# Optimization experiments

Measured on AMD Instinct MI355X. Metric: run time of the kernel, lower is better.

The kernel has to match this reference:

```python
import jax, jax.numpy as jnp
import numpy as np

Tx, V, D = 512, 100, 64
DM, NH, DFF, NL = 512, 8, 2048, 2
H, DATT, FCH, OUT = 256, 128, 256, 2


def setup_inputs() -> dict:
    key = jax.random.key(0)
    ks = jax.random.split(key, 16)
    s = 0.02
    w = lambda k, shape: jax.random.normal(k, shape, jnp.float32) * s
    return dict(
        x_data=jax.random.normal(ks[0], (1, Tx, V, D), jnp.float32),
        feat_w=w(ks[1], (DM, D)), feat_b=jnp.zeros((DM,), jnp.float32),
        in_w=w(ks[2], (NL, 3 * DM, DM)), in_b=jnp.zeros((NL, 3 * DM), jnp.float32),
        out_w=w(ks[3], (NL, DM, DM)), out_b=jnp.zeros((NL, DM), jnp.float32),
        ff1_w=w(ks[4], (NL, DFF, DM)), ff1_b=jnp.zeros((NL, DFF), jnp.float32),
        ff2_w=w(ks[5], (NL, DM, DFF)), ff2_b=jnp.zeros((NL, DM), jnp.float32),
        ln1_g=jnp.ones((NL, DM), jnp.float32), ln1_b=jnp.zeros((NL, DM), jnp.float32),
        ln2_g=jnp.ones((NL, DM), jnp.float32), ln2_b=jnp.zeros((NL, DM), jnp.float32),
        att1_w=w(ks[6], (DATT, DM + H)), att1_b=jnp.zeros((DATT,), jnp.float32),
        att2_w=w(ks[7], (1, DATT)), att2_b=jnp.zeros((1,), jnp.float32),
        lstm_wih=w(ks[8], (4 * H, DM)), lstm_whh=w(ks[9], (4 * H, H)),
        lstm_bih=jnp.zeros((4 * H,), jnp.float32), lstm_bhh=jnp.zeros((4 * H,), jnp.float32),
        fc1_w=w(ks[10], (FCH, DM + H)), fc1_b=jnp.zeros((FCH,), jnp.float32),
        fc2_w=w(ks[11], (OUT, FCH)), fc2_b=jnp.zeros((OUT,), jnp.float32),
    )


def _layernorm(x, g, b):
    m = x.mean(-1, keepdims=True)
    v = x.var(-1, keepdims=True)
    return (x - m) * jax.lax.rsqrt(v + 1e-5) * g + b


def _forward(x_data, feat_w, feat_b, in_w, in_b, out_w, out_b, ff1_w, ff1_b,
             ff2_w, ff2_b, ln1_g, ln1_b, ln2_g, ln2_b, att1_w, att1_b,
             att2_w, att2_b, lstm_wih, lstm_whh, lstm_bih, lstm_bhh,
             fc1_w, fc1_b, fc2_w, fc2_b):
    x = x_data[0]                              # [Tx, V, D]
    x = jnp.swapaxes(x, 0, 1)                  # [V, Tx, D]  (seq=V, batch=Tx)
    x = x @ feat_w.T + feat_b                  # feature mapping -> [V, Tx, DM]
    # sinusoidal positional encoding over the V (seq) axis
    pos = jnp.arange(V, dtype=jnp.float32)[:, None]
    div = jnp.exp(jnp.arange(0, DM, 2, dtype=jnp.float32) * (-np.log(10000.0) / DM))
    pe = jnp.zeros((V, DM), jnp.float32)
    pe = pe.at[:, 0::2].set(jnp.sin(pos * div)).at[:, 1::2].set(jnp.cos(pos * div))
    x = x + pe[:, None, :]
    hd = DM // NH
    for l in range(NL):                        # post-norm TransformerEncoderLayer
        qkv = x @ in_w[l].T + in_b[l]          # [V, Tx, 3*DM]
        q, k, v = jnp.split(qkv, 3, axis=-1)
        q = q.reshape(V, Tx, NH, hd)
        k = k.reshape(V, Tx, NH, hd)
        v = v.reshape(V, Tx, NH, hd)
        scores = jnp.einsum('ibhd,jbhd->bhij', q, k) / np.sqrt(hd).astype(np.float32)
        attn = jax.nn.softmax(scores, axis=-1)
        ctx = jnp.einsum('bhij,jbhd->ibhd', attn, v).reshape(V, Tx, DM)
        x = _layernorm(x + ctx @ out_w[l].T + out_b[l], ln1_g[l], ln1_b[l])
        ff = jax.nn.relu(x @ ff1_w[l].T + ff1_b[l]) @ ff2_w[l].T + ff2_b[l]
        x = _layernorm(x + ff, ln2_g[l], ln2_b[l])
    hs = jnp.swapaxes(x, 0, 1)                 # [Tx, V, DM]

    def step(carry, h_i):                      # h_i: [V, DM]
        s_h, s_c = carry                       # [1, H] each
        att_in = jnp.concatenate([h_i, jnp.broadcast_to(s_h, (V, H))], axis=1)
        a1 = jnp.tanh(att_in @ att1_w.T + att1_b)
        a2 = a1 @ att2_w.T + att2_b            # [V, 1]
        a2 = a2 - jnp.max(a2)
        alpha = jnp.exp(a2)
        alpha = alpha / (jnp.sum(alpha, axis=0, keepdims=True) + 1e-15)
        c = jnp.sum(alpha * h_i, axis=0, keepdims=True)   # [1, DM]
        gates = c @ lstm_wih.T + lstm_bih + s_h @ lstm_whh.T + lstm_bhh
        i_g, f_g, g_g, o_g = jnp.split(gates, 4, axis=-1)
        s_c_new = jax.nn.sigmoid(f_g) * s_c + jax.nn.sigmoid(i_g) * jnp.tanh(g_g)
        s_h_new = jax.nn.sigmoid(o_g) * jnp.tanh(s_c_new)
        fc_in = jnp.concatenate([c, s_h], axis=1)  # uses PREVIOUS hidden, per original
        fc = jax.nn.relu(fc_in @ fc1_w.T + fc1_b) @ fc2_w.T + fc2_b
        log_prob = jax.nn.log_softmax(fc, axis=1)  # [1, OUT]
        return (s_h_new, s_c_new), log_prob

    init = (jnp.zeros((1, H), jnp.float32), jnp.zeros((1, H), jnp.float32))
    _, logs = jax.lax.scan(step, init, hs)
    return logs[-1]                            # last timestep's log-probs [1, OUT]


def reference(x_data, feat_w, feat_b, in_w, in_b, out_w, out_b, ff1_w, ff1_b,
              ff2_w, ff2_b, ln1_g, ln1_b, ln2_g, ln2_b, att1_w, att1_b,
              att2_w, att2_b, lstm_wih, lstm_whh, lstm_bih, lstm_bhh,
              fc1_w, fc1_b, fc2_w, fc2_b):
    return _forward(x_data, feat_w, feat_b, in_w, in_b, out_w, out_b, ff1_w,
                    ff1_b, ff2_w, ff2_b, ln1_g, ln1_b, ln2_g, ln2_b, att1_w,
                    att1_b, att2_w, att2_b, lstm_wih, lstm_whh, lstm_bih,
                    lstm_bhh, fc1_w, fc1_b, fc2_w, fc2_b)
```

## Files before the change

kernel.cpp:

```cpp
#include <hip/hip_runtime.h>
#include <hip/hip_bf16.h>


typedef __attribute__((ext_vector_type(8))) short short8;
typedef __attribute__((ext_vector_type(4))) float f32x4;

__device__ __forceinline__ int jglob_of(int e0, int jl) { return ((jl >> 4) << 8) + e0 + (jl & 15); }
__device__ __forceinline__ float blo(unsigned u) { return __uint_as_float(u << 16); }
__device__ __forceinline__ float bhi(unsigned u) { return __uint_as_float(u & 0xffff0000u); }
__device__ __forceinline__ short f2bs(float x) {
  union { __hip_bfloat16 h; short s; } u; u.h = __float2bfloat16(x); return u.s;
}
__device__ __forceinline__ float tanhf_fast(float x) {
  float e = __expf(2.f * x);
  return 1.f - 2.f * __builtin_amdgcn_rcpf(e + 1.f);
}

#define GLL16(GSRC, LDST) \
  __builtin_amdgcn_global_load_lds( \
      (const __attribute__((address_space(1))) unsigned int*)(GSRC), \
      (__attribute__((address_space(3))) unsigned int*)(LDST), 16, 0, 0)

__global__ __launch_bounds__(256) void pe_kernel(float* __restrict__ pe) {
  int idx = blockIdx.x * 256 + threadIdx.x;
  if (idx >= 100 * 512) return;
  int v = idx >> 9, n = idx & 511;
  float d = expf(-(float)(n & ~1) * (9.2103403719761836f / 512.0f));
  float ang = (float)v * d;
  pe[idx] = (n & 1) ? cosf(ang) : sinf(ang);
}

__global__ __launch_bounds__(256) void cvt_kernel(const float* __restrict__ src,
                                                  __hip_bfloat16* __restrict__ dst, int n) {
  int i = blockIdx.x * 256 + threadIdx.x;
  if (i < n) dst[i] = __float2bfloat16(src[i]);
}

__global__ __launch_bounds__(256) void gemm_bf16(
    const __hip_bfloat16* __restrict__ A, long aBase, int aDiv, long aSA, long aSB,
    const __hip_bfloat16* __restrict__ W, int ldw,
    const float* __restrict__ bias,
    float* __restrict__ outF, __hip_bfloat16* __restrict__ outB,
    long oBase, int oDiv, long oSA, long oSB,
    int K, int addTo, int relu)
{
  __shared__ __hip_bfloat16 As[128 * 64];
  __shared__ __hip_bfloat16 Bs[128 * 64];
  const int tid = threadIdx.x;
  const int rT = blockIdx.y * 128, nT = blockIdx.x * 128;
  const int wave = tid >> 6, lane = tid & 63;
  const int wr = wave >> 1, wc = wave & 1;
  const int lrow = lane & 15, lkg = lane >> 4;

  long asrc[4], bsrc[4];
  const int sc8 = ((lane & 7) ^ (lane >> 3)) * 8;
#pragma unroll
  for (int i = 0; i < 4; ++i) {
    const int chunk = wave * 4 + i;
    const int row = chunk * 8 + (lane >> 3);
    const int gr = rT + row;
    asrc[i] = aBase + (long)(gr / aDiv) * aSA + (long)(gr % aDiv) * aSB + sc8;
    bsrc[i] = (long)(nT + row) * ldw + sc8;
  }

  f32x4 acc[4][4];
#pragma unroll
  for (int i = 0; i < 4; ++i)
#pragma unroll
    for (int j = 0; j < 4; ++j) acc[i][j] = (f32x4){0.f, 0.f, 0.f, 0.f};

  for (int k0 = 0; k0 < K; k0 += 64) {
#pragma unroll
    for (int i = 0; i < 4; ++i) {
      const int chunk = wave * 4 + i;
      GLL16(A + asrc[i] + k0, &As[chunk * 512]);
      GLL16(W + bsrc[i] + k0, &Bs[chunk * 512]);
    }
    __syncthreads();
#pragma unroll
    for (int ks = 0; ks < 2; ++ks) {
      short8 af[4], bfv[4];
#pragma unroll
      for (int f = 0; f < 4; ++f) {
        const int Ra = wr * 64 + f * 16 + lrow;
        af[f] = *(const short8*)&As[Ra * 64 + (((ks * 4 + lkg) ^ (Ra & 7)) * 8)];
        const int Rb = wc * 64 + f * 16 + lrow;
        bfv[f] = *(const short8*)&Bs[Rb * 64 + (((ks * 4 + lkg) ^ (Rb & 7)) * 8)];
      }
#pragma unroll
      for (int fm = 0; fm < 4; ++fm)
#pragma unroll
        for (int fn = 0; fn < 4; ++fn)
          acc[fm][fn] = __builtin_amdgcn_mfma_f32_16x16x32_bf16(af[fm], bfv[fn], acc[fm][fn], 0, 0, 0);
    }
    __syncthreads();
  }

  float bias_v[4];
#pragma unroll
  for (int fn = 0; fn < 4; ++fn)
    bias_v[fn] = bias ? bias[nT + wc * 64 + fn * 16 + lrow] : 0.f;

#pragma unroll
  for (int fm = 0; fm < 4; ++fm) {
#pragma unroll
    for (int r = 0; r < 4; ++r) {
      const int grow = rT + wr * 64 + fm * 16 + lkg * 4 + r;
      const long obase_r = oBase + (long)(grow / oDiv) * oSA + (long)(grow % oDiv) * oSB;
#pragma unroll
      for (int fn = 0; fn < 4; ++fn) {
        const int gcol = nT + wc * 64 + fn * 16 + lrow;
        float v = acc[fm][fn][r] + bias_v[fn];
        if (relu) v = fmaxf(v, 0.f);
        const long o = obase_r + gcol;
        if (outF) { if (addTo) v += outF[o]; outF[o] = v; }
        else outB[o] = __float2bfloat16(v);
      }
    }
  }
}

__global__ __launch_bounds__(256) void gemm_mfma(
    const float* __restrict__ A, long aBase, int aDiv, long aSA, long aSB,
    const float* __restrict__ W, int ldw,
    const float* __restrict__ bias,
    const float* __restrict__ extra, int extraDiv,
    float* __restrict__ outF, __hip_bfloat16* __restrict__ outB,
    __hip_bfloat16* __restrict__ outB2,
    long oBase, int oDiv, long oSA, long oSB, long oSC,
    int N, int K, int addTo, int relu)
{
  __shared__ short As[2][128][40];
  __shared__ short Bs[2][128][40];
  const int tid = threadIdx.x;
  const int rT = blockIdx.y * 128, nT = blockIdx.x * 128;
  const int wave = tid >> 6, lane = tid & 63;
  const int wr = wave >> 1, wc = wave & 1;
  const int lrow = lane & 15, lkg = lane >> 4;
  const int srow = tid >> 1, shf = tid & 1;

  const long arow = aBase + (long)((rT + srow) / aDiv) * aSA + (long)((rT + srow) % aDiv) * aSB + shf * 16;
  const long brow = (long)(nT + srow) * ldw + shf * 16;

  f32x4 acc[4][4];
#pragma unroll
  for (int i = 0; i < 4; ++i)
#pragma unroll
    for (int j = 0; j < 4; ++j) acc[i][j] = (f32x4){0.f, 0.f, 0.f, 0.f};

  float4 ra[4], rb[4];
#define LOADT(K0) do { \
    const float* _pa = A + arow + (K0); \
    ra[0] = *(const float4*)(_pa); ra[1] = *(const float4*)(_pa + 4); \
    ra[2] = *(const float4*)(_pa + 8); ra[3] = *(const float4*)(_pa + 12); \
    const float* _pb = W + brow + (K0); \
    rb[0] = *(const float4*)(_pb); rb[1] = *(const float4*)(_pb + 4); \
    rb[2] = *(const float4*)(_pb + 8); rb[3] = *(const float4*)(_pb + 12); \
  } while (0)

#define CVST(DST, X, Y) do { \
    short8 _v; \
    _v[0] = f2bs((X).x); _v[1] = f2bs((X).y); _v[2] = f2bs((X).z); _v[3] = f2bs((X).w); \
    _v[4] = f2bs((Y).x); _v[5] = f2bs((Y).y); _v[6] = f2bs((Y).z); _v[7] = f2bs((Y).w); \
    *(short8*)(DST) = _v; \
  } while (0)

#define STAGE(BUF) do { \
    CVST(&As[BUF][srow][shf * 16],     ra[0], ra[1]); \
    CVST(&As[BUF][srow][shf * 16 + 8], ra[2], ra[3]); \
    CVST(&Bs[BUF][srow][shf * 16],     rb[0], rb[1]); \
    CVST(&Bs[BUF][srow][shf * 16 + 8], rb[2], rb[3]); \
  } while (0)

  LOADT(0);
  STAGE(0);
  __syncthreads();

  int cur = 0;
  for (int k0 = 0; k0 < K; k0 += 32) {
    const bool nlast = (k0 + 32 < K);
    if (nlast) LOADT(k0 + 32);
    short8 af[4], bfv[4];
#pragma unroll
    for (int f = 0; f < 4; ++f)
      af[f] = *(const short8*)&As[cur][wr * 64 + f * 16 + lrow][lkg * 8];
#pragma unroll
    for (int f = 0; f < 4; ++f)
      bfv[f] = *(const short8*)&Bs[cur][wc * 64 + f * 16 + lrow][lkg * 8];
#pragma unroll
    for (int fm = 0; fm < 4; ++fm)
#pragma unroll
      for (int fn = 0; fn < 4; ++fn)
        acc[fm][fn] = __builtin_amdgcn_mfma_f32_16x16x32_bf16(af[fm], bfv[fn], acc[fm][fn], 0, 0, 0);
    if (nlast) STAGE(cur ^ 1);
    __syncthreads();
    cur ^= 1;
  }

  float bias_v[4];
#pragma unroll
  for (int fn = 0; fn < 4; ++fn)
    bias_v[fn] = bias ? bias[nT + wc * 64 + fn * 16 + lrow] : 0.f;

#pragma unroll
  for (int fm = 0; fm < 4; ++fm) {
#pragma unroll
    for (int r = 0; r < 4; ++r) {
      const int grow = rT + wr * 64 + fm * 16 + lkg * 4 + r;
      const long obase_r = oBase + (long)(grow / oDiv) * oSA + (long)(grow % oDiv) * oSB;
      const long exrow = (long)(grow / extraDiv) * N;
#pragma unroll
      for (int fn = 0; fn < 4; ++fn) {
        const int gcol = nT + wc * 64 + fn * 16 + lrow;
        float v = acc[fm][fn][r] + bias_v[fn];
        if (extra) v += extra[exrow + gcol];
        if (relu) v = fmaxf(v, 0.f);
        const long o = obase_r + (long)gcol * oSC;
        if (outF) { if (addTo) v += outF[o]; outF[o] = v; }
        else outB[o] = __float2bfloat16(v);
        if (outB2) outB2[o] = __float2bfloat16(v);
      }
    }
  }
#undef LOADT
#undef CVST
#undef STAGE
}

__global__ __launch_bounds__(256) void attn_kernel(
    const __hip_bfloat16* __restrict__ qkv, __hip_bfloat16* __restrict__ outY)
{
  __shared__ __align__(16) char arena[101632];
  unsigned short* Qs = (unsigned short*)arena;
  unsigned short* Ks = Qs + 8064;
  unsigned short* Vt = Ks + 8064;
  float* S = (float*)(arena + 49664);
  unsigned short* Sb = (unsigned short*)arena;
  __shared__ float rs_s[112];

  const int h = blockIdx.x, bl = blockIdx.y, tid = threadIdx.x;
  const unsigned short* q16 = (const unsigned short*)qkv;

  for (int idx = tid; idx < 6400; idx += 256) {
    int v = idx >> 6, d = idx & 63;
    long base = ((long)(v * 128 + bl)) * 1536 + h * 64 + d;
    Qs[v * 72 + d] = q16[base];
    Ks[v * 72 + d] = q16[base + 512];
    Vt[d * 136 + v] = q16[base + 1024];
  }
  for (int idx = tid; idx < 12 * 64; idx += 256) {
    int r = 100 + (idx >> 6), c = idx & 63;
    Qs[r * 72 + c] = 0; Ks[r * 72 + c] = 0;
  }
  for (int idx = tid; idx < 64 * 36; idx += 256) {
    int d = idx / 36, c = 100 + idx % 36;
    Vt[d * 136 + c] = 0;
  }
  __syncthreads();

  const int wave = tid >> 6, lane = tid & 63;
  const int lrow = lane & 15, lkg = lane >> 4;

  for (int tt = wave; tt < 49; tt += 4) {
    const int tm = tt / 7, tn = tt % 7;
    f32x4 a = (f32x4){0.f, 0.f, 0.f, 0.f};
#pragma unroll
    for (int ks = 0; ks < 2; ++ks) {
      short8 af = *(const short8*)&Qs[(tm * 16 + lrow) * 72 + ks * 32 + lkg * 8];
      short8 bf = *(const short8*)&Ks[(tn * 16 + lrow) * 72 + ks * 32 + lkg * 8];
      a = __builtin_amdgcn_mfma_f32_16x16x32_bf16(af, bf, a, 0, 0, 0);
    }
#pragma unroll
    for (int r = 0; r < 4; ++r)
      S[(tm * 16 + lkg * 4 + r) * 116 + tn * 16 + lrow] = a[r] * 0.125f;
  }
  __syncthreads();

  {
    unsigned* p = (unsigned*)Sb;
    for (int idx = tid; idx < 7616; idx += 256) p[idx] = 0;
  }
  __syncthreads();

  if (tid < 200) {
    const int r = tid >> 1, hf = tid & 1;
    const float* srow = S + r * 116 + hf * 50;
    float m = -3.0e38f;
    for (int c = 0; c < 50; ++c) m = fmaxf(m, srow[c]);
    m = fmaxf(m, __shfl_xor(m, 1, 64));
    float s = 0.f;
    for (int c = 0; c < 50; ++c) {
      float e = __expf(srow[c] - m);
      Sb[r * 136 + hf * 50 + c] = (unsigned short)f2bs(e);
      s += e;
    }
    s += __shfl_xor(s, 1, 64);
    if (hf == 0) rs_s[r] = 1.f / s;
  }
  __syncthreads();

  for (int tt = wave; tt < 28; tt += 4) {
    const int tm = tt >> 2, tn = tt & 3;
    f32x4 a = (f32x4){0.f, 0.f, 0.f, 0.f};
#pragma unroll
    for (int kc = 0; kc < 4; ++kc) {
      short8 af = *(const short8*)&Sb[(tm * 16 + lrow) * 136 + kc * 32 + lkg * 8];
      short8 bf = *(const short8*)&Vt[(tn * 16 + lrow) * 136 + kc * 32 + lkg * 8];
      a = __builtin_amdgcn_mfma_f32_16x16x32_bf16(af, bf, a, 0, 0, 0);
    }
#pragma unroll
    for (int r = 0; r < 4; ++r) {
      const int m = tm * 16 + lkg * 4 + r;
      if (m < 100) {
        const int n = tn * 16 + lrow;
        outY[((long)m * 128 + bl) * 512 + h * 64 + n] = __float2bfloat16(a[r] * rs_s[m]);
      }
    }
  }
}

__global__ __launch_bounds__(256) void ln_kernel(float* __restrict__ X,
    __hip_bfloat16* __restrict__ Xb,
    const float* __restrict__ g, const float* __restrict__ b)
{
  const int row = blockIdx.x * 4 + (threadIdx.x >> 6);
  const int lane = threadIdx.x & 63;
  float* x = X + (long)row * 512;
  __hip_bfloat16* xb = Xb + (long)row * 512;
  float v[8]; float s = 0.f, sq = 0.f;
#pragma unroll
  for (int i = 0; i < 8; ++i) { v[i] = x[lane + i * 64]; s += v[i]; sq += v[i] * v[i]; }
#pragma unroll
  for (int off = 32; off; off >>= 1) { s += __shfl_xor(s, off, 64); sq += __shfl_xor(sq, off, 64); }
  const float mean = s * (1.f / 512.f);
  const float var = sq * (1.f / 512.f) - mean * mean;
  const float inv = rsqrtf(var + 1e-5f);
#pragma unroll
  for (int i = 0; i < 8; ++i) {
    int c = lane + i * 64;
    float r = (v[i] - mean) * inv * g[c] + b[c];
    x[c] = r;
    xb[c] = __float2bfloat16(r);
  }
}

__global__ void init_kernel(unsigned long long* sh_units, float* c_g) {
  int t = threadIdx.x;
  sh_units[t] = 0ULL;
  sh_units[256 + t] = 0ULL;
  c_g[t] = 0.f; c_g[256 + t] = 0.f;
}

#define DEC_NB 16

__global__ __launch_bounds__(256, 1) void decoder_kernel(
    const float* __restrict__ X,
    const __hip_bfloat16* __restrict__ Pb,
    const __hip_bfloat16* __restrict__ Gb,
    const float* __restrict__ att1_w, const float* __restrict__ att1_b,
    const float* __restrict__ att2_w,
    const float* __restrict__ whh,
    const float* __restrict__ bih, const float* __restrict__ bhh,
    const float* __restrict__ fc1_w, const float* __restrict__ fc1_b,
    const float* __restrict__ fc2_w, const float* __restrict__ fc2_b,
    unsigned long long* sh_units,
    float* c_g,
    float* __restrict__ out)
{
  if (blockIdx.x & 7) return;
  const int tid = threadIdx.x;
  const int blk = blockIdx.x >> 3;
  const int e0 = blk * 16;

  __shared__ __align__(16) float s_h_s[256];
  __shared__ float w2_s[128], ub_s[128], bsum_s[64];
  __shared__ float u_s[128], sc_s[16];
  __shared__ float a2_s[104];
  __shared__ float red_s[256];
  __shared__ float gates_s[64];
  __shared__ float red4_s[4];
  __shared__ float fcin_s[768];
  __shared__ float fca_s[256];

  if (tid < 128) { w2_s[tid] = att2_w[tid]; ub_s[tid] = att1_b[tid]; }
  if (tid < 64) {
    int jg = jglob_of(e0, tid);
    bsum_s[tid] = bih[jg] + bhh[jg];
  }
  if (tid < 16) sc_s[tid] = 0.f;
  if (tid < 4) a2_s[100 + tid] = 0.f;

  const int pv = tid >> 1, ppart = tid & 1;
  const int pvv = (pv < 100) ? pv : 99;
  const int gjl = tid >> 2, gq = tid & 3;
  const long gRowOff = (long)jglob_of(e0, gjl) * 100 + gq * 26;

  unsigned W1R[64];
  {
    const int j = tid >> 1, hf = tid & 1;
    const float* wsrc = att1_w + (long)j * 768 + 512 + hf * 128;
#pragma unroll
    for (int i = 0; i < 64; ++i)
      W1R[i] = (unsigned)(unsigned short)f2bs(wsrc[2 * i]) |
               ((unsigned)(unsigned short)f2bs(wsrc[2 * i + 1]) << 16);
  }
  float WHF[64];
  {
    const float* wsrc = whh + (long)jglob_of(e0, gjl) * 256 + gq * 64;
#pragma unroll
    for (int i = 0; i < 64; ++i) WHF[i] = wsrc[i];
  }

  unsigned PCa[32], PCb[32];
  unsigned GCa[13], GCb[13];

#define PREFETCH(T1, PCd, GCd) do { \
    const uint4* _pp = (const uint4*)Pb + ((((long)(T1) * 100 + pvv) * 128 + ppart * 64) >> 3); \
    _Pragma("unroll") \
    for (int _i = 0; _i < 8; ++_i) { \
      uint4 _t = _pp[_i]; \
      (PCd)[4*_i] = _t.x; (PCd)[4*_i+1] = _t.y; (PCd)[4*_i+2] = _t.z; (PCd)[4*_i+3] = _t.w; \
    } \
    const unsigned* _gp = (const unsigned*)(Gb + (long)(T1) * 102400 + gRowOff); \
    _Pragma("unroll") \
    for (int _i = 0; _i < 13; ++_i) (GCd)[_i] = _gp[_i]; \
  } while (0)

#define STEP(T, PCc, GCc, PCn, GCn) do { \
     \
    { \
      unsigned long long* _up = &sh_units[((((T) & 1) ^ 1) << 8) + tid]; \
      unsigned long long _v = __hip_atomic_load(_up, __ATOMIC_RELAXED, __HIP_MEMORY_SCOPE_AGENT); \
      while ((unsigned)(_v >> 32) < (unsigned)(T)) { \
        __builtin_amdgcn_s_sleep(1); \
        _v = __hip_atomic_load(_up, __ATOMIC_RELAXED, __HIP_MEMORY_SCOPE_AGENT); \
      } \
      s_h_s[tid] = __uint_as_float((unsigned)_v); \
    } \
    __syncthreads(); \
     \
    if ((T) + 1 < 512) PREFETCH((T) + 1, PCn, GCn); \
     \
    { const int _hf = tid & 1, _j = tid >> 1; \
      const float* _sh = &s_h_s[_hf * 128]; \
      float _a = 0.f; \
      _Pragma("unroll") \
      for (int _i = 0; _i < 64; ++_i) { \
        const unsigned _w = W1R[_i]; \
        const float2 _s2 = *(const float2*)(_sh + 2 * _i); \
        _a += blo(_w) * _s2.x + bhi(_w) * _s2.y; \
      } \
      _a += __shfl_xor(_a, 1, 64); \
      if (_hf == 0) u_s[_j] = _a + ub_s[_j]; \
    } \
    float _hhv; \
    { const float* _sh = &s_h_s[gq * 64]; \
      float _a = 0.f; \
      _Pragma("unroll") \
      for (int _i = 0; _i < 16; ++_i) { \
        const float4 _s4 = *(const float4*)(_sh + 4 * _i); \
        _a += WHF[4*_i] * _s4.x + WHF[4*_i+1] * _s4.y + WHF[4*_i+2] * _s4.z + WHF[4*_i+3] * _s4.w; \
      } \
      _a += __shfl_xor(_a, 1, 64); \
      _a += __shfl_xor(_a, 2, 64); \
      _hhv = _a; \
    } \
    __syncthreads(); \
     \
    { float _val = 0.f; \
      _Pragma("unroll") \
      for (int _jj = 0; _jj < 64; ++_jj) { \
        unsigned _u = (PCc)[_jj >> 1]; \
        float _pf = (_jj & 1) ? bhi(_u) : blo(_u); \
        int _col = ppart * 64 + _jj; \
        _val += tanhf_fast(_pf + u_s[_col]) * w2_s[_col]; \
      } \
      _val += __shfl_xor(_val, 1, 64); \
      if (ppart == 0 && pv < 100) a2_s[pv] = _val; \
    } \
    __syncthreads(); \
     \
    if (tid < 64) { \
      float _x0 = a2_s[tid]; \
      float _x1 = (tid + 64 < 100) ? a2_s[tid + 64] : -3.0e38f; \
      float _m = fmaxf(_x0, _x1); \
      _Pragma("unroll") \
      for (int _o = 32; _o; _o >>= 1) _m = fmaxf(_m, __shfl_xor(_m, _o, 64)); \
      float _e0 = __expf(_x0 - _m); \
      float _e1 = (tid + 64 < 100) ? __expf(_x1 - _m) : 0.f; \
      float _s = _e0 + _e1; \
      _Pragma("unroll") \
      for (int _o = 32; _o; _o >>= 1) _s += __shfl_xor(_s, _o, 64); \
      const float _inv = 1.f / (_s + 1e-15f); \
      a2_s[tid] = _e0 * _inv; \
      if (tid + 64 < 100) a2_s[tid + 64] = _e1 * _inv; \
    } \
    __syncthreads(); \
     \
    { float _p = 0.f; \
      _Pragma("unroll") \
      for (int _i = 0; _i < 13; ++_i) { \
        unsigned _u = (GCc)[_i]; \
        _p += a2_s[gq * 26 + 2 * _i] * blo(_u); \
        _p += a2_s[gq * 26 + 2 * _i + 1] * bhi(_u); \
      } \
      _p += __shfl_xor(_p, 1, 64); \
      _p += __shfl_xor(_p, 2, 64); \
      if (gq == 0) gates_s[gjl] = _p + _hhv + bsum_s[gjl]; \
    } \
    __syncthreads(); \
     \
    if ((T) < 511) { \
      if (tid < 16) { \
        const float _ig = gates_s[tid], _fg = gates_s[16 + tid]; \
        const float _gg = gates_s[32 + tid], _og = gates_s[48 + tid]; \
        const float _si = 1.f / (1.f + __expf(-_ig)); \
        const float _sf = 1.f / (1.f + __expf(-_fg)); \
        const float _so = 1.f / (1.f + __expf(-_og)); \
        const float _sc = _sf * sc_s[tid] + _si * tanhf(_gg); \
        sc_s[tid] = _sc; \
        const float _sh2 = _so * tanhf(_sc); \
        const unsigned long long _v = \
            ((unsigned long long)(unsigned)((T) + 1) << 32) | (unsigned long long)__float_as_uint(_sh2); \
        __hip_atomic_store(&sh_units[(((T) & 1) << 8) + e0 + tid], _v, \
                           __ATOMIC_RELAXED, __HIP_MEMORY_SCOPE_AGENT); \
      } \
    } else { \
      const int _dl = tid & 31, _vs = tid >> 5; \
      const int _v0 = _vs * 13, _v1 = (_v0 + 13 < 100) ? _v0 + 13 : 100; \
      float _ac = 0.f; \
      for (int _v = _v0; _v < _v1; ++_v) \
        _ac += a2_s[_v] * X[((long)(_v * 512 + 511)) * 512 + blk * 32 + _dl]; \
      red_s[tid] = _ac; \
      __syncthreads(); \
      if (tid < 32) { \
        float _cc = 0.f; \
        _Pragma("unroll") \
        for (int _s = 0; _s < 8; ++_s) _cc += red_s[_s * 32 + tid]; \
        __hip_atomic_store(&c_g[blk * 32 + tid], _cc, __ATOMIC_RELAXED, __HIP_MEMORY_SCOPE_AGENT); \
      } \
      __syncthreads(); \
      if (tid == 0) \
        __hip_atomic_store(&sh_units[256 + e0], 512ULL << 32, \
                           __ATOMIC_RELEASE, __HIP_MEMORY_SCOPE_AGENT); \
    } \
  } while (0)

  PREFETCH(0, PCa, GCa);
  __syncthreads();

  for (int t2 = 0; t2 < 512; t2 += 2) {
    STEP(t2,     PCa, GCa, PCb, GCb);
    STEP(t2 + 1, PCb, GCb, PCa, GCa);
  }

  if (blk == 0) {
    if (tid < DEC_NB) {
      while ((unsigned)(__hip_atomic_load(&sh_units[256 + tid * 16],
                 __ATOMIC_RELAXED, __HIP_MEMORY_SCOPE_AGENT) >> 32) < 512u)
        __builtin_amdgcn_s_sleep(1);
    }
    __builtin_amdgcn_fence(__ATOMIC_ACQUIRE, "agent");
    __syncthreads();
    fcin_s[tid]       = __hip_atomic_load(&c_g[tid],       __ATOMIC_RELAXED, __HIP_MEMORY_SCOPE_AGENT);
    fcin_s[256 + tid] = __hip_atomic_load(&c_g[256 + tid], __ATOMIC_RELAXED, __HIP_MEMORY_SCOPE_AGENT);
    fcin_s[512 + tid] = s_h_s[tid];
    __syncthreads();
    float acc = fc1_b[tid];
    const float* w = fc1_w + (long)tid * 768;
    for (int k = 0; k < 768; ++k) acc += w[k] * fcin_s[k];
    fca_s[tid] = fmaxf(acc, 0.f);
    __syncthreads();
    if (tid < 128) {
      const int r = tid >> 6, k0 = tid & 63;
      float a = 0.f;
#pragma unroll
      for (int s = 0; s < 4; ++s) a += fc2_w[r * 256 + k0 + s * 64] * fca_s[k0 + s * 64];
#pragma unroll
      for (int off = 32; off; off >>= 1) a += __shfl_xor(a, off, 64);
      if (k0 == 0) red4_s[r] = a + fc2_b[r];
    }
    __syncthreads();
    if (tid == 0) {
      const float l0 = red4_s[0], l1 = red4_s[1];
      const float m = fmaxf(l0, l1);
      const float ls = logf(__expf(l0 - m) + __expf(l1 - m));
      out[0] = l0 - m - ls;
      out[1] = l1 - m - ls;
    }
  }
#undef PREFETCH
#undef STEP
}

extern "C" void kernel_launch(void* const* d_in, const int* in_sizes, int n_in,
                              void* d_out, int out_size, void* d_ws, size_t ws_size,
                              hipStream_t stream) {
  const float* x_data  = (const float*)d_in[0];
  const float* feat_w  = (const float*)d_in[1];
  const float* feat_b  = (const float*)d_in[2];
  const float* in_w    = (const float*)d_in[3];
  const float* in_b    = (const float*)d_in[4];
  const float* out_w   = (const float*)d_in[5];
  const float* out_b   = (const float*)d_in[6];
  const float* ff1_w   = (const float*)d_in[7];
  const float* ff1_b   = (const float*)d_in[8];
  const float* ff2_w   = (const float*)d_in[9];
  const float* ff2_b   = (const float*)d_in[10];
  const float* ln1_g   = (const float*)d_in[11];
  const float* ln1_b   = (const float*)d_in[12];
  const float* ln2_g   = (const float*)d_in[13];
  const float* ln2_b   = (const float*)d_in[14];
  const float* att1_w  = (const float*)d_in[15];
  const float* att1_b  = (const float*)d_in[16];
  const float* att2_w  = (const float*)d_in[17];
  const float* lstm_wih = (const float*)d_in[19];
  const float* lstm_whh = (const float*)d_in[20];
  const float* lstm_bih = (const float*)d_in[21];
  const float* lstm_bhh = (const float*)d_in[22];
  const float* fc1_w   = (const float*)d_in[23];
  const float* fc1_b   = (const float*)d_in[24];
  const float* fc2_w   = (const float*)d_in[25];
  const float* fc2_b   = (const float*)d_in[26];

  float* ws   = (float*)d_ws;
  float* Xf   = ws;
  float* R    = Xf + 26214400;
  __hip_bfloat16* Xb   = (__hip_bfloat16*)R;
  __hip_bfloat16* qkvb = (__hip_bfloat16*)(R + 13107200);
  __hip_bfloat16* ctxb = (__hip_bfloat16*)(R + 22937600);
  __hip_bfloat16* ffh  = (__hip_bfloat16*)(R + 13107200);
  __hip_bfloat16* wb   = (__hip_bfloat16*)(R + 26214400);
  __hip_bfloat16* in_wb  = wb;
  __hip_bfloat16* out_wb = wb + 1572864;
  __hip_bfloat16* ff1_wb = out_wb + 524288;
  __hip_bfloat16* ff2_wb = ff1_wb + 2097152;
  __hip_bfloat16* PbB = (__hip_bfloat16*)R;
  __hip_bfloat16* GbB = (__hip_bfloat16*)(R + 3276800);
  float* pe    = R + 29491200;
  unsigned long long* sh_units = (unsigned long long*)(pe + 51200);
  float* c_g   = (float*)(sh_units + 512);

  pe_kernel<<<200, 256, 0, stream>>>(pe);
  cvt_kernel<<<(1572864 + 255) / 256, 256, 0, stream>>>(in_w, in_wb, 1572864);
  cvt_kernel<<<(524288 + 255) / 256, 256, 0, stream>>>(out_w, out_wb, 524288);
  cvt_kernel<<<(2097152 + 255) / 256, 256, 0, stream>>>(ff1_w, ff1_wb, 2097152);
  cvt_kernel<<<(2097152 + 255) / 256, 256, 0, stream>>>(ff2_w, ff2_wb, 2097152);

  gemm_mfma<<<dim3(4, 400), 256, 0, stream>>>(
      x_data, 0L, 512, 64L, 6400L, feat_w, 64, feat_b, pe, 512,
      Xf, nullptr, Xb, 0L, 1 << 30, 0L, 512L, 1L, 512, 64, 0, 0);

  for (int l = 0; l < 2; ++l) {
    for (int c = 0; c < 4; ++c) {
      const long b0 = c * 128;
      gemm_bf16<<<dim3(12, 100), 256, 0, stream>>>(
          Xb, b0 * 512, 128, 262144L, 512L,
          in_wb + (long)l * 786432, 512, in_b + l * 1536,
          nullptr, qkvb, 0L, 1 << 30, 0L, 1536L, 512, 0, 0);
      attn_kernel<<<dim3(8, 128), 256, 0, stream>>>(qkvb, ctxb);
      gemm_bf16<<<dim3(4, 100), 256, 0, stream>>>(
          ctxb, 0L, 1 << 30, 0L, 512L,
          out_wb + (long)l * 262144, 512, out_b + l * 512,
          Xf, nullptr, b0 * 512, 128, 262144L, 512L, 512, 1, 0);
    }
    ln_kernel<<<12800, 256, 0, stream>>>(Xf, Xb, ln1_g + l * 512, ln1_b + l * 512);
    for (int rc = 0; rc < 4; ++rc) {
      const long r0 = (long)rc * 12800;
      gemm_bf16<<<dim3(16, 100), 256, 0, stream>>>(
          Xb, r0 * 512, 1 << 30, 0L, 512L,
          ff1_wb + (long)l * 1048576, 512, ff1_b + l * 2048,
          nullptr, ffh, 0L, 1 << 30, 0L, 2048L, 512, 0, 1);
      gemm_bf16<<<dim3(4, 100), 256, 0, stream>>>(
          ffh, 0L, 1 << 30, 0L, 2048L,
          ff2_wb + (long)l * 1048576, 2048, ff2_b + l * 512,
          Xf, nullptr, r0 * 512, 1 << 30, 0L, 512L, 2048, 1, 0);
    }
    ln_kernel<<<12800, 256, 0, stream>>>(Xf, Xb, ln2_g + l * 512, ln2_b + l * 512);
  }

  gemm_mfma<<<dim3(1, 400), 256, 0, stream>>>(
      Xf, 0L, 100, 512L, 262144L, att1_w, 768, nullptr, nullptr, 1,
      nullptr, PbB, nullptr, 0L, 1 << 30, 0L, 128L, 1L, 128, 512, 0, 0);
  gemm_mfma<<<dim3(8, 400), 256, 0, stream>>>(
      Xf, 0L, 100, 512L, 262144L, lstm_wih, 512, nullptr, nullptr, 1,
      nullptr, GbB, nullptr, 0L, 100, 102400L, 1L, 100L, 1024, 512, 0, 0);

  init_kernel<<<1, 256, 0, stream>>>(sh_units, c_g);
  decoder_kernel<<<DEC_NB * 8, 256, 0, stream>>>(
      Xf, PbB, GbB, att1_w, att1_b, att2_w,
      lstm_whh, lstm_bih, lstm_bhh, fc1_w, fc1_b, fc2_w, fc2_b,
      sh_units, c_g, (float*)d_out);
}
```

Before: 5.339 ms.

## Keep residual stream in bf16 only and batch attention/GEMM chunks larger

Removes the fp32 residual buffer so the whole encoder stream lives in bf16. Residual adds in the GEMM epilogues and layernorm now read and write bf16, with vectorized 16-byte layernorm access. Attention and FFN chunks double in size, the out-projection runs once per layer, and the post-encoder projections use the bf16 GEMM with pre-converted weights. This cuts memory traffic and launch count but adds bf16 rounding to every residual update, which may hurt accuracy.

```diff
diff --git a/kernel.cpp b/kernel.cpp
--- a/kernel.cpp
+++ b/kernel.cpp
@@ -30,10 +30,11 @@
   pe[idx] = (n & 1) ? cosf(ang) : sinf(ang);
 }
 
-__global__ __launch_bounds__(256) void cvt_kernel(const float* __restrict__ src,
-                                                  __hip_bfloat16* __restrict__ dst, int n) {
+__global__ __launch_bounds__(256) void cvt2_kernel(const float* __restrict__ src,
+                                                   __hip_bfloat16* __restrict__ dst,
+                                                   int n, int w, int stride) {
   int i = blockIdx.x * 256 + threadIdx.x;
-  if (i < n) dst[i] = __float2bfloat16(src[i]);
+  if (i < n) dst[i] = __float2bfloat16(src[(i / w) * stride + (i % w)]);
 }
 
 __global__ __launch_bounds__(256) void gemm_bf16(
@@ -41,7 +42,7 @@
     const __hip_bfloat16* __restrict__ W, int ldw,
     const float* __restrict__ bias,
     float* __restrict__ outF, __hip_bfloat16* __restrict__ outB,
-    long oBase, int oDiv, long oSA, long oSB,
+    long oBase, int oDiv, long oSA, long oSB, long oSC,
     int K, int addTo, int relu)
 {
   __shared__ __hip_bfloat16 As[128 * 64];
@@ -112,9 +113,12 @@
         const int gcol = nT + wc * 64 + fn * 16 + lrow;
         float v = acc[fm][fn][r] + bias_v[fn];
         if (relu) v = fmaxf(v, 0.f);
-        const long o = obase_r + gcol;
+        const long o = obase_r + (long)gcol * oSC;
         if (outF) { if (addTo) v += outF[o]; outF[o] = v; }
-        else outB[o] = __float2bfloat16(v);
+        else {
+          if (addTo) v += __bfloat162float(outB[o]);
+          outB[o] = __float2bfloat16(v);
+        }
       }
     }
   }
@@ -125,10 +129,9 @@
     const float* __restrict__ W, int ldw,
     const float* __restrict__ bias,
     const float* __restrict__ extra, int extraDiv,
-    float* __restrict__ outF, __hip_bfloat16* __restrict__ outB,
-    __hip_bfloat16* __restrict__ outB2,
-    long oBase, int oDiv, long oSA, long oSB, long oSC,
-    int N, int K, int addTo, int relu)
+    __hip_bfloat16* __restrict__ outB,
+    long oBase, int oDiv, long oSA, long oSB,
+    int N, int K)
 {
   __shared__ short As[2][128][40];
   __shared__ short Bs[2][128][40];
@@ -214,11 +217,7 @@
         const int gcol = nT + wc * 64 + fn * 16 + lrow;
         float v = acc[fm][fn][r] + bias_v[fn];
         if (extra) v += extra[exrow + gcol];
-        if (relu) v = fmaxf(v, 0.f);
-        const long o = obase_r + (long)gcol * oSC;
-        if (outF) { if (addTo) v += outF[o]; outF[o] = v; }
-        else outB[o] = __float2bfloat16(v);
-        if (outB2) outB2[o] = __float2bfloat16(v);
+        outB[obase_r + gcol] = __float2bfloat16(v);
       }
     }
   }
@@ -228,7 +227,7 @@
 }
 
 __global__ __launch_bounds__(256) void attn_kernel(
-    const __hip_bfloat16* __restrict__ qkv, __hip_bfloat16* __restrict__ outY)
+    const __hip_bfloat16* __restrict__ qkv, __hip_bfloat16* __restrict__ outY, int b0)
 {
   __shared__ __align__(16) char arena[101632];
   unsigned short* Qs = (unsigned short*)arena;
@@ -243,7 +242,7 @@
 
   for (int idx = tid; idx < 6400; idx += 256) {
     int v = idx >> 6, d = idx & 63;
-    long base = ((long)(v * 128 + bl)) * 1536 + h * 64 + d;
+    long base = ((long)(v * 256 + bl)) * 1536 + h * 64 + d;
     Qs[v * 72 + d] = q16[base];
     Ks[v * 72 + d] = q16[base + 512];
     Vt[d * 136 + v] = q16[base + 1024];
@@ -313,35 +312,36 @@
       const int m = tm * 16 + lkg * 4 + r;
       if (m < 100) {
         const int n = tn * 16 + lrow;
-        outY[((long)m * 128 + bl) * 512 + h * 64 + n] = __float2bfloat16(a[r] * rs_s[m]);
+        outY[((long)(m * 512 + b0 + bl)) * 512 + h * 64 + n] = __float2bfloat16(a[r] * rs_s[m]);
       }
     }
   }
 }
 
-__global__ __launch_bounds__(256) void ln_kernel(float* __restrict__ X,
-    __hip_bfloat16* __restrict__ Xb,
+__global__ __launch_bounds__(256) void ln_kernel(__hip_bfloat16* __restrict__ X,
     const float* __restrict__ g, const float* __restrict__ b)
 {
   const int row = blockIdx.x * 4 + (threadIdx.x >> 6);
   const int lane = threadIdx.x & 63;
-  float* x = X + (long)row * 512;
-  __hip_bfloat16* xb = Xb + (long)row * 512;
-  float v[8]; float s = 0.f, sq = 0.f;
-#pragma unroll
-  for (int i = 0; i < 8; ++i) { v[i] = x[lane + i * 64]; s += v[i]; sq += v[i] * v[i]; }
+  unsigned short* x = (unsigned short*)X + (long)row * 512 + lane * 8;
+  uint4 raw = *(const uint4*)x;
+  float v[8];
+  v[0] = blo(raw.x); v[1] = bhi(raw.x); v[2] = blo(raw.y); v[3] = bhi(raw.y);
+  v[4] = blo(raw.z); v[5] = bhi(raw.z); v[6] = blo(raw.w); v[7] = bhi(raw.w);
+  float s = 0.f, sq = 0.f;
+#pragma unroll
+  for (int i = 0; i < 8; ++i) { s += v[i]; sq += v[i] * v[i]; }
 #pragma unroll
   for (int off = 32; off; off >>= 1) { s += __shfl_xor(s, off, 64); sq += __shfl_xor(sq, off, 64); }
   const float mean = s * (1.f / 512.f);
   const float var = sq * (1.f / 512.f) - mean * mean;
   const float inv = rsqrtf(var + 1e-5f);
-#pragma unroll
-  for (int i = 0; i < 8; ++i) {
-    int c = lane + i * 64;
-    float r = (v[i] - mean) * inv * g[c] + b[c];
-    x[c] = r;
-    xb[c] = __float2bfloat16(r);
-  }
+  const int c0 = lane * 8;
+  short8 outv;
+#pragma unroll
+  for (int i = 0; i < 8; ++i)
+    outv[i] = f2bs((v[i] - mean) * inv * g[c0 + i] + b[c0 + i]);
+  *(short8*)x = outv;
 }
 
 __global__ void init_kernel(unsigned long long* sh_units, float* c_g) {
@@ -354,7 +354,7 @@
 #define DEC_NB 16
 
 __global__ __launch_bounds__(256, 1) void decoder_kernel(
-    const float* __restrict__ X,
+    const __hip_bfloat16* __restrict__ Xb,
     const __hip_bfloat16* __restrict__ Pb,
     const __hip_bfloat16* __restrict__ Gb,
     const float* __restrict__ att1_w, const float* __restrict__ att1_b,
@@ -427,7 +427,6 @@
   } while (0)
 
 #define STEP(T, PCc, GCc, PCn, GCn) do { \
-     \
     { \
       unsigned long long* _up = &sh_units[((((T) & 1) ^ 1) << 8) + tid]; \
       unsigned long long _v = __hip_atomic_load(_up, __ATOMIC_RELAXED, __HIP_MEMORY_SCOPE_AGENT); \
@@ -438,9 +437,7 @@
       s_h_s[tid] = __uint_as_float((unsigned)_v); \
     } \
     __syncthreads(); \
-     \
     if ((T) + 1 < 512) PREFETCH((T) + 1, PCn, GCn); \
-     \
     { const int _hf = tid & 1, _j = tid >> 1; \
       const float* _sh = &s_h_s[_hf * 128]; \
       float _a = 0.f; \
@@ -466,7 +463,6 @@
       _hhv = _a; \
     } \
     __syncthreads(); \
-     \
     { float _val = 0.f; \
       _Pragma("unroll") \
       for (int _jj = 0; _jj < 64; ++_jj) { \
@@ -479,7 +475,6 @@
       if (ppart == 0 && pv < 100) a2_s[pv] = _val; \
     } \
     __syncthreads(); \
-     \
     if (tid < 64) { \
       float _x0 = a2_s[tid]; \
       float _x1 = (tid + 64 < 100) ? a2_s[tid + 64] : -3.0e38f; \
@@ -496,7 +491,6 @@
       if (tid + 64 < 100) a2_s[tid + 64] = _e1 * _inv; \
     } \
     __syncthreads(); \
-     \
     { float _p = 0.f; \
       _Pragma("unroll") \
       for (int _i = 0; _i < 13; ++_i) { \
@@ -509,7 +503,6 @@
       if (gq == 0) gates_s[gjl] = _p + _hhv + bsum_s[gjl]; \
     } \
     __syncthreads(); \
-     \
     if ((T) < 511) { \
       if (tid < 16) { \
         const float _ig = gates_s[tid], _fg = gates_s[16 + tid]; \
@@ -530,7 +523,7 @@
       const int _v0 = _vs * 13, _v1 = (_v0 + 13 < 100) ? _v0 + 13 : 100; \
       float _ac = 0.f; \
       for (int _v = _v0; _v < _v1; ++_v) \
-        _ac += a2_s[_v] * X[((long)(_v * 512 + 511)) * 512 + blk * 32 + _dl]; \
+        _ac += a2_s[_v] * __bfloat162float(Xb[((long)(_v * 512 + 511)) * 512 + blk * 32 + _dl]); \
       red_s[tid] = _ac; \
       __syncthreads(); \
       if (tid < 32) { \
@@ -624,71 +617,74 @@
   const float* fc2_b   = (const float*)d_in[26];
 
   float* ws   = (float*)d_ws;
-  float* Xf   = ws;
-  float* R    = Xf + 26214400;
-  __hip_bfloat16* Xb   = (__hip_bfloat16*)R;
-  __hip_bfloat16* qkvb = (__hip_bfloat16*)(R + 13107200);
-  __hip_bfloat16* ctxb = (__hip_bfloat16*)(R + 22937600);
-  __hip_bfloat16* ffh  = (__hip_bfloat16*)(R + 13107200);
-  __hip_bfloat16* wb   = (__hip_bfloat16*)(R + 26214400);
-  __hip_bfloat16* in_wb  = wb;
-  __hip_bfloat16* out_wb = wb + 1572864;
-  __hip_bfloat16* ff1_wb = out_wb + 524288;
-  __hip_bfloat16* ff2_wb = ff1_wb + 2097152;
-  __hip_bfloat16* PbB = (__hip_bfloat16*)R;
-  __hip_bfloat16* GbB = (__hip_bfloat16*)(R + 3276800);
-  float* pe    = R + 29491200;
+  __hip_bfloat16* Xb = (__hip_bfloat16*)ws;
+  float* R2   = ws + 13107200;
+  __hip_bfloat16* qkvb = (__hip_bfloat16*)R2;
+  __hip_bfloat16* ctxb = (__hip_bfloat16*)(R2 + 19660800);
+  __hip_bfloat16* ffh  = (__hip_bfloat16*)R2;
+  __hip_bfloat16* PbB  = (__hip_bfloat16*)R2;
+  __hip_bfloat16* GbB  = (__hip_bfloat16*)(R2 + 3276800);
+  __hip_bfloat16* wbp  = (__hip_bfloat16*)(R2 + 32768000);
+  __hip_bfloat16* in_wb  = wbp;
+  __hip_bfloat16* out_wb = wbp + 1572864;
+  __hip_bfloat16* ff1_wb = wbp + 2097152;
+  __hip_bfloat16* ff2_wb = wbp + 4194304;
+  __hip_bfloat16* att1c  = wbp + 6291456;
+  __hip_bfloat16* wih_b  = wbp + 6356992;
+  float* pe    = R2 + 32768000 + 3440640;
   unsigned long long* sh_units = (unsigned long long*)(pe + 51200);
   float* c_g   = (float*)(sh_units + 512);
 
   pe_kernel<<<200, 256, 0, stream>>>(pe);
-  cvt_kernel<<<(1572864 + 255) / 256, 256, 0, stream>>>(in_w, in_wb, 1572864);
-  cvt_kernel<<<(524288 + 255) / 256, 256, 0, stream>>>(out_w, out_wb, 524288);
-  cvt_kernel<<<(2097152 + 255) / 256, 256, 0, stream>>>(ff1_w, ff1_wb, 2097152);
-  cvt_kernel<<<(2097152 + 255) / 256, 256, 0, stream>>>(ff2_w, ff2_wb, 2097152);
+  cvt2_kernel<<<(1572864 + 255) / 256, 256, 0, stream>>>(in_w, in_wb, 1572864, 512, 512);
+  cvt2_kernel<<<(524288 + 255) / 256, 256, 0, stream>>>(out_w, out_wb, 524288, 512, 512);
+  cvt2_kernel<<<(2097152 + 255) / 256, 256, 0, stream>>>(ff1_w, ff1_wb, 2097152, 512, 512);
+  cvt2_kernel<<<(2097152 + 255) / 256, 256, 0, stream>>>(ff2_w, ff2_wb, 2097152, 2048, 2048);
+  cvt2_kernel<<<(65536 + 255) / 256, 256, 0, stream>>>(att1_w, att1c, 65536, 512, 768);
+  cvt2_kernel<<<(524288 + 255) / 256, 256, 0, stream>>>(lstm_wih, wih_b, 524288, 512, 512);
 
   gemm_mfma<<<dim3(4, 400), 256, 0, stream>>>(
       x_data, 0L, 512, 64L, 6400L, feat_w, 64, feat_b, pe, 512,
-      Xf, nullptr, Xb, 0L, 1 << 30, 0L, 512L, 1L, 512, 64, 0, 0);
+      Xb, 0L, 1 << 30, 0L, 512L, 512, 64);
 
   for (int l = 0; l < 2; ++l) {
-    for (int c = 0; c < 4; ++c) {
-      const long b0 = c * 128;
-      gemm_bf16<<<dim3(12, 100), 256, 0, stream>>>(
-          Xb, b0 * 512, 128, 262144L, 512L,
+    for (int c = 0; c < 2; ++c) {
+      const long b0 = c * 256;
+      gemm_bf16<<<dim3(12, 200), 256, 0, stream>>>(
+          Xb, b0 * 512, 256, 262144L, 512L,
           in_wb + (long)l * 786432, 512, in_b + l * 1536,
-          nullptr, qkvb, 0L, 1 << 30, 0L, 1536L, 512, 0, 0);
-      attn_kernel<<<dim3(8, 128), 256, 0, stream>>>(qkvb, ctxb);
-      gemm_bf16<<<dim3(4, 100), 256, 0, stream>>>(
-          ctxb, 0L, 1 << 30, 0L, 512L,
-          out_wb + (long)l * 262144, 512, out_b + l * 512,
-          Xf, nullptr, b0 * 512, 128, 262144L, 512L, 512, 1, 0);
-    }
-    ln_kernel<<<12800, 256, 0, stream>>>(Xf, Xb, ln1_g + l * 512, ln1_b + l * 512);
-    for (int rc = 0; rc < 4; ++rc) {
-      const long r0 = (long)rc * 12800;
-      gemm_bf16<<<dim3(16, 100), 256, 0, stream>>>(
+          nullptr, qkvb, 0L, 1 << 30, 0L, 1536L, 1L, 512, 0, 0);
+      attn_kernel<<<dim3(8, 256), 256, 0, stream>>>(qkvb, ctxb, (int)b0);
+    }
+    gemm_bf16<<<dim3(4, 400), 256, 0, stream>>>(
+        ctxb, 0L, 1 << 30, 0L, 512L,
+        out_wb + (long)l * 262144, 512, out_b + l * 512,
+        nullptr, Xb, 0L, 1 << 30, 0L, 512L, 1L, 512, 1, 0);
+    ln_kernel<<<12800, 256, 0, stream>>>(Xb, ln1_g + l * 512, ln1_b + l * 512);
+    for (int rc = 0; rc < 2; ++rc) {
+      const long r0 = (long)rc * 25600;
+      gemm_bf16<<<dim3(16, 200), 256, 0, stream>>>(
           Xb, r0 * 512, 1 << 30, 0L, 512L,
           ff1_wb + (long)l * 1048576, 512, ff1_b + l * 2048,
-          nullptr, ffh, 0L, 1 << 30, 0L, 2048L, 512, 0, 1);
-      gemm_bf16<<<dim3(4, 100), 256, 0, stream>>>(
+          nullptr, ffh, 0L, 1 << 30, 0L, 2048L, 1L, 512, 0, 1);
+      gemm_bf16<<<dim3(4, 200), 256, 0, stream>>>(
           ffh, 0L, 1 << 30, 0L, 2048L,
           ff2_wb + (long)l * 1048576, 2048, ff2_b + l * 512,
-          Xf, nullptr, r0 * 512, 1 << 30, 0L, 512L, 2048, 1, 0);
-    }
-    ln_kernel<<<12800, 256, 0, stream>>>(Xf, Xb, ln2_g + l * 512, ln2_b + l * 512);
-  }
-
-  gemm_mfma<<<dim3(1, 400), 256, 0, stream>>>(
-      Xf, 0L, 100, 512L, 262144L, att1_w, 768, nullptr, nullptr, 1,
-      nullptr, PbB, nullptr, 0L, 1 << 30, 0L, 128L, 1L, 128, 512, 0, 0);
-  gemm_mfma<<<dim3(8, 400), 256, 0, stream>>>(
-      Xf, 0L, 100, 512L, 262144L, lstm_wih, 512, nullptr, nullptr, 1,
-      nullptr, GbB, nullptr, 0L, 100, 102400L, 1L, 100L, 1024, 512, 0, 0);
+          nullptr, Xb, r0 * 512, 1 << 30, 0L, 512L, 1L, 2048, 1, 0);
+    }
+    ln_kernel<<<12800, 256, 0, stream>>>(Xb, ln2_g + l * 512, ln2_b + l * 512);
+  }
+
+  gemm_bf16<<<dim3(1, 400), 256, 0, stream>>>(
+      Xb, 0L, 100, 512L, 262144L, att1c, 512, nullptr,
+      nullptr, PbB, 0L, 1 << 30, 0L, 128L, 1L, 512, 0, 0);
+  gemm_bf16<<<dim3(8, 400), 256, 0, stream>>>(
+      Xb, 0L, 100, 512L, 262144L, wih_b, 512, nullptr,
+      nullptr, GbB, 0L, 100, 102400L, 1L, 100L, 512, 0, 0);
 
   init_kernel<<<1, 256, 0, stream>>>(sh_units, c_g);
   decoder_kernel<<<DEC_NB * 8, 256, 0, stream>>>(
-      Xf, PbB, GbB, att1_w, att1_b, att2_w,
+      Xb, PbB, GbB, att1_w, att1_b, att2_w,
       lstm_whh, lstm_bih, lstm_bhh, fc1_w, fc1_b, fc2_w, fc2_b,
       sh_units, c_g, (float*)d_out);
 }
```

After: 4.884 ms. 8.5% less time.
